# Kernel optimization log

Hardware: AMD Instinct MI355X
Metric: run time of the kernel (lower is better)

Reference implementation:

```python
import jax, jax.numpy as jnp
import numpy as np

B = 8          # batch of protein states
N = 20000      # num_nodes (atoms)
D = 640        # input_dim (latent per atom)
R = 2500       # number of residues (segments)
BINS = 10      # output_size_per_segment = (1, 10)
HID = 128      # decoder hidden dim
COND = 3       # conditioner_mode='X_ref' -> 3D reference coords
EPS = 1e-5     # BatchNorm1d eps


def _make_res_id():
    # ragged residue sizes cycling [6,8,10,8] -> exactly R residues, N atoms
    sizes = np.tile(np.array([6, 8, 10, 8], dtype=np.int64), R // 4)
    assert sizes.sum() == N
    return jnp.asarray(np.repeat(np.arange(R), sizes), dtype=jnp.int32)


def setup_inputs() -> dict:
    key = jax.random.key(0)
    ks = jax.random.split(key, 6)
    x = jax.random.normal(ks[0], (B * N, D), dtype=jnp.float32)
    conditioner = jax.random.normal(ks[1], (N, COND), dtype=jnp.float32)
    res_id = _make_res_id()  # [N] int32, sorted, atom -> residue
    W1 = jax.random.normal(ks[2], (BINS + COND, HID), dtype=jnp.float32) * 0.2
    b1 = jnp.zeros((HID,), jnp.float32)
    gamma = jnp.ones((HID,), jnp.float32)
    beta = jnp.zeros((HID,), jnp.float32)
    W2 = jax.random.normal(ks[3], (HID, 3), dtype=jnp.float32) * 0.1
    b2 = jnp.zeros((3,), jnp.float32)
    return {"x": x, "conditioner": conditioner, "res_id": res_id,
            "W1": W1, "b1": b1, "gamma": gamma, "beta": beta,
            "W2": W2, "b2": b2}


def reference(x, conditioner, res_id, W1, b1, gamma, beta, W2, b2):
    # x: [B*N, D] -> [B, N, D]
    x3 = x.reshape(B, N, D)

    # --- fused per-residue AdaptiveAvgPool2d((1,10)) ---
    # H-axis (atoms in residue) -> 1 : ragged segment mean via segment_sum
    counts = jax.ops.segment_sum(jnp.ones((N,), x.dtype), res_id,
                                 num_segments=R)                  # [R]
    seg_sum = jax.vmap(
        lambda xb: jax.ops.segment_sum(xb, res_id, num_segments=R)
    )(x3)                                                          # [B, R, D]
    seg_mean = seg_sum / counts[None, :, None]
    # W-axis: D -> 10 adaptive bins (exact since D % 10 == 0)
    pooled_latent = seg_mean.reshape(B, R, BINS, D // BINS).mean(-1)  # [B,R,10]

    # expand residue pooled vector back to its atoms, concat conditioner
    per_atom = pooled_latent[:, res_id, :]                        # [B, N, 10]
    cond = jnp.broadcast_to(conditioner[None], (B, N, COND))      # [B, N, 3]
    feat = jnp.concatenate([per_atom, cond], axis=-1).reshape(B * N, BINS + COND)

    # --- decoder MLP: Linear -> ReLU -> BatchNorm1d (train stats) -> Linear ---
    h = jax.nn.relu(feat @ W1 + b1)                               # [B*N, 128]
    mu = h.mean(axis=0)
    var = ((h - mu) ** 2).mean(axis=0)                            # biased, as torch BN
    hn = (h - mu) * jax.lax.rsqrt(var + EPS) * gamma + beta
    out = hn @ W2 + b2                                            # [B*N, 3]
    return out.reshape(B, N, 3)
```

## Files before the change

### kernel.cpp

```cpp
#include <hip/hip_runtime.h>

#define BB    8
#define NN    20000
#define DD    640
#define RR    2500
#define NBINS 10
#define HID   128
#define MTOT  (BB*NN)
#define SBLK  2048

__global__ void seg_bounds_kernel(const int* __restrict__ res_id,
                                  int* __restrict__ seg_start) {
    int r = blockIdx.x * blockDim.x + threadIdx.x;
    if (r > RR) return;
    if (r == RR) { seg_start[RR] = NN; return; }
    int lo = 0, hi = NN;
    while (lo < hi) {
        int mid = (lo + hi) >> 1;
        if (res_id[mid] < r) lo = mid + 1; else hi = mid;
    }
    seg_start[r] = lo;
}

__global__ __launch_bounds__(640) void pool_kernel(const float* __restrict__ x,
                                                   const int* __restrict__ seg_start,
                                                   float* __restrict__ pooled) {
    __shared__ float sbin[NBINS];
    int br = blockIdx.x;
    int b = br / RR;
    int r = br - b * RR;
    int t = threadIdx.x;
    if (t < NBINS) sbin[t] = 0.f;
    __syncthreads();

    int s0  = seg_start[r];
    int cnt = seg_start[r + 1] - s0;
    int nf4 = (cnt * DD) >> 2;
    const float4* xp = (const float4*)(x + (size_t)(b * NN + s0) * DD);

    float sum = 0.f;
    for (int idx = t; idx < nf4; idx += 640) {
        float4 v = xp[idx];
        sum += (v.x + v.y) + (v.z + v.w);
    }

    sum += __shfl_down(sum, 8, 16);
    sum += __shfl_down(sum, 4, 16);
    sum += __shfl_down(sum, 2, 16);
    sum += __shfl_down(sum, 1, 16);
    if ((t & 15) == 0) {
        int bin = ((t << 2) % DD) >> 6;
        atomicAdd(&sbin[bin], sum);
    }
    __syncthreads();
    if (t < NBINS) {
        float inv = cnt > 0 ? 1.f / (64.f * (float)cnt) : 0.f;
        pooled[(size_t)(b * RR + r) * NBINS + t] = sbin[t] * inv;
    }
}

__global__ __launch_bounds__(128) void stats_kernel(const float* __restrict__ pooled,
                                                    const float* __restrict__ cond,
                                                    const int* __restrict__ res_id,
                                                    const float* __restrict__ W1,
                                                    const float* __restrict__ b1,
                                                    float* __restrict__ partial) {
    int k = threadIdx.x;
    float w[13];
    #pragma unroll
    for (int j = 0; j < 13; j++) w[j] = W1[j * HID + k];
    float bk = b1[k];

    float s = 0.f, s2 = 0.f;
    for (int i = blockIdx.x; i < MTOT; i += SBLK) {
        int b = i / NN;
        int n = i - b * NN;
        int rid = res_id[n];
        const float* pr = pooled + (size_t)(b * RR + rid) * NBINS;
        const float* cr = cond + (size_t)n * 3;
        float h = bk;
        #pragma unroll
        for (int j = 0; j < NBINS; j++) h = fmaf(pr[j], w[j], h);
        h = fmaf(cr[0], w[10], h);
        h = fmaf(cr[1], w[11], h);
        h = fmaf(cr[2], w[12], h);
        h = fmaxf(h, 0.f);
        s += h;
        s2 = fmaf(h, h, s2);
    }
    partial[blockIdx.x * 256 + k]       = s;
    partial[blockIdx.x * 256 + 128 + k] = s2;
}

__global__ __launch_bounds__(1024) void finalize_kernel(const float* __restrict__ partial,
                                                        const float* __restrict__ gamma,
                                                        const float* __restrict__ beta,
                                                        const float* __restrict__ W2,
                                                        const float* __restrict__ b2,
                                                        float* __restrict__ W2eff,
                                                        float* __restrict__ b2eff) {
    int t = threadIdx.x;
    int slot = t & 255;
    int grp  = t >> 8;
    float acc = 0.f;
    for (int bi = grp; bi < SBLK; bi += 4) acc += partial[bi * 256 + slot];

    __shared__ float part4[4][256];
    __shared__ float contrib[HID * 3];
    part4[grp][slot] = acc;
    __syncthreads();

    if (t < HID) {
        float s  = part4[0][t] + part4[1][t] + part4[2][t] + part4[3][t];
        float s2 = part4[0][128 + t] + part4[1][128 + t] + part4[2][128 + t] + part4[3][128 + t];
        const float invM = 1.f / (float)MTOT;
        float mu  = s * invM;
        float var = fmaxf(s2 * invM - mu * mu, 0.f);
        float rs  = rsqrtf(var + 1e-5f);
        float sc  = gamma[t] * rs;
        float tk  = beta[t] - mu * sc;
        #pragma unroll
        for (int j = 0; j < 3; j++) {
            float wv = W2[t * 3 + j];
            W2eff[t * 3 + j]   = sc * wv;
            contrib[t * 3 + j] = tk * wv;
        }
    }
    __syncthreads();
    if (t < 3) {
        float a2 = b2[t];
        for (int kk = 0; kk < HID; kk++) a2 += contrib[kk * 3 + t];
        b2eff[t] = a2;
    }
}

__global__ __launch_bounds__(256) void out_kernel(const float* __restrict__ pooled,
                                                  const float* __restrict__ cond,
                                                  const int* __restrict__ res_id,
                                                  const float* __restrict__ W1,
                                                  const float* __restrict__ b1,
                                                  const float* __restrict__ W2eff,
                                                  const float* __restrict__ b2eff,
                                                  float* __restrict__ out) {
    int lane = threadIdx.x & 63;
    int wid  = (blockIdx.x * blockDim.x + threadIdx.x) >> 6;
    int nw   = (gridDim.x * blockDim.x) >> 6;
    int k1 = lane, k2 = lane + 64;

    float wa[13], wb[13];
    #pragma unroll
    for (int j = 0; j < 13; j++) {
        wa[j] = W1[j * HID + k1];
        wb[j] = W1[j * HID + k2];
    }
    float b1a = b1[k1], b1b = b1[k2];
    float wa0 = W2eff[k1 * 3 + 0], wa1 = W2eff[k1 * 3 + 1], wa2 = W2eff[k1 * 3 + 2];
    float wb0 = W2eff[k2 * 3 + 0], wb1 = W2eff[k2 * 3 + 1], wb2 = W2eff[k2 * 3 + 2];
    float e0 = b2eff[0], e1 = b2eff[1], e2 = b2eff[2];

    for (int i = wid; i < MTOT; i += nw) {
        int b = i / NN;
        int n = i - b * NN;
        int rid = res_id[n];
        const float* pr = pooled + (size_t)(b * RR + rid) * NBINS;
        const float* cr = cond + (size_t)n * 3;

        float h1 = b1a, h2 = b1b;
        #pragma unroll
        for (int j = 0; j < NBINS; j++) {
            h1 = fmaf(pr[j], wa[j], h1);
            h2 = fmaf(pr[j], wb[j], h2);
        }
        h1 = fmaf(cr[0], wa[10], h1); h1 = fmaf(cr[1], wa[11], h1); h1 = fmaf(cr[2], wa[12], h1);
        h2 = fmaf(cr[0], wb[10], h2); h2 = fmaf(cr[1], wb[11], h2); h2 = fmaf(cr[2], wb[12], h2);
        h1 = fmaxf(h1, 0.f);
        h2 = fmaxf(h2, 0.f);

        float p0 = h1 * wa0 + h2 * wb0;
        float p1 = h1 * wa1 + h2 * wb1;
        float p2 = h1 * wa2 + h2 * wb2;
        #pragma unroll
        for (int m = 1; m < 64; m <<= 1) {
            p0 += __shfl_xor(p0, m, 64);
            p1 += __shfl_xor(p1, m, 64);
            p2 += __shfl_xor(p2, m, 64);
        }
        if (lane == 0) {
            out[(size_t)i * 3 + 0] = p0 + e0;
            out[(size_t)i * 3 + 1] = p1 + e1;
            out[(size_t)i * 3 + 2] = p2 + e2;
        }
    }
}

extern "C" void kernel_launch(void* const* d_in, const int* in_sizes, int n_in,
                              void* d_out, int out_size, void* d_ws, size_t ws_size,
                              hipStream_t stream) {
    const float* x      = (const float*)d_in[0];
    const float* cond   = (const float*)d_in[1];
    const int*   res_id = (const int*)  d_in[2];
    const float* W1     = (const float*)d_in[3];
    const float* b1     = (const float*)d_in[4];
    const float* gamma  = (const float*)d_in[5];
    const float* beta   = (const float*)d_in[6];
    const float* W2     = (const float*)d_in[7];
    const float* b2     = (const float*)d_in[8];
    float* out = (float*)d_out;

    char* w = (char*)d_ws;
    int*   seg_start = (int*)  (w);
    float* pooled    = (float*)(w + 16384);
    float* partial   = (float*)(w + (1 << 20));
    float* W2eff     = (float*)(w + (3 << 20));
    float* b2eff     = (float*)(w + (3 << 20) + 4096);

    hipLaunchKernelGGL(seg_bounds_kernel, dim3(10), dim3(256), 0, stream,
                       res_id, seg_start);
    hipLaunchKernelGGL(pool_kernel, dim3(BB * RR), dim3(640), 0, stream,
                       x, seg_start, pooled);
    hipLaunchKernelGGL(stats_kernel, dim3(SBLK), dim3(128), 0, stream,
                       pooled, cond, res_id, W1, b1, partial);
    hipLaunchKernelGGL(finalize_kernel, dim3(1), dim3(1024), 0, stream,
                       partial, gamma, beta, W2, b2, W2eff, b2eff);
    hipLaunchKernelGGL(out_kernel, dim3(1024), dim3(256), 0, stream,
                       pooled, cond, res_id, W1, b1, W2eff, b2eff, out);
}
```

Baseline: 784.5 us.

## Map one row per thread in output MLP, fold segment bounds into pooling

The output kernel now assigns one atom row to each thread, with W1, W2eff and b1 staged in shared memory. Each thread recomputes the full 128-wide hidden layer itself, which removes the per-row 64-lane shuffle reductions and the 2/3-idle lane-0 stores. The separate segment-bounds kernel is removed; each pool block now binary-searches its own bounds, saving one launch at the cost of redundant searches. The stats grid also shrinks from 2048 to 1024 blocks, leaving fewer partials to reduce.

```diff
diff --git a/kernel.cpp b/kernel.cpp
--- a/kernel.cpp
+++ b/kernel.cpp
@@ -7,34 +7,32 @@
 #define NBINS 10
 #define HID   128
 #define MTOT  (BB*NN)
-#define SBLK  2048
-
-__global__ void seg_bounds_kernel(const int* __restrict__ res_id,
-                                  int* __restrict__ seg_start) {
-    int r = blockIdx.x * blockDim.x + threadIdx.x;
-    if (r > RR) return;
-    if (r == RR) { seg_start[RR] = NN; return; }
-    int lo = 0, hi = NN;
-    while (lo < hi) {
-        int mid = (lo + hi) >> 1;
-        if (res_id[mid] < r) lo = mid + 1; else hi = mid;
-    }
-    seg_start[r] = lo;
-}
+#define SBLK  1024
+#define OSTR  20
 
 __global__ __launch_bounds__(640) void pool_kernel(const float* __restrict__ x,
-                                                   const int* __restrict__ seg_start,
+                                                   const int* __restrict__ res_id,
                                                    float* __restrict__ pooled) {
     __shared__ float sbin[NBINS];
+    __shared__ int sbounds[2];
     int br = blockIdx.x;
     int b = br / RR;
     int r = br - b * RR;
     int t = threadIdx.x;
     if (t < NBINS) sbin[t] = 0.f;
-    __syncthreads();
-
-    int s0  = seg_start[r];
-    int cnt = seg_start[r + 1] - s0;
+    if (t < 2) {
+        int target = r + t;
+        int lo = 0, hi = NN;
+        while (lo < hi) {
+            int mid = (lo + hi) >> 1;
+            if (res_id[mid] < target) lo = mid + 1; else hi = mid;
+        }
+        sbounds[t] = lo;
+    }
+    __syncthreads();
+
+    int s0  = sbounds[0];
+    int cnt = sbounds[1] - s0;
     int nf4 = (cnt * DD) >> 2;
     const float4* xp = (const float4*)(x + (size_t)(b * NN + s0) * DD);
 
@@ -142,55 +140,47 @@
                                                   const float* __restrict__ W2eff,
                                                   const float* __restrict__ b2eff,
                                                   float* __restrict__ out) {
-    int lane = threadIdx.x & 63;
-    int wid  = (blockIdx.x * blockDim.x + threadIdx.x) >> 6;
-    int nw   = (gridDim.x * blockDim.x) >> 6;
-    int k1 = lane, k2 = lane + 64;
-
-    float wa[13], wb[13];
+    __shared__ float sw[HID * OSTR];
+    __shared__ float sb2[3];
+    int t = threadIdx.x;
+    for (int k = t; k < HID; k += 256) {
+        #pragma unroll
+        for (int j = 0; j < 13; j++) sw[k * OSTR + j] = W1[j * HID + k];
+        sw[k * OSTR + 13] = W2eff[k * 3 + 0];
+        sw[k * OSTR + 14] = W2eff[k * 3 + 1];
+        sw[k * OSTR + 15] = W2eff[k * 3 + 2];
+        sw[k * OSTR + 16] = b1[k];
+    }
+    if (t < 3) sb2[t] = b2eff[t];
+    __syncthreads();
+
+    int i = blockIdx.x * 256 + t;
+    int b = i / NN;
+    int n = i - b * NN;
+    int rid = res_id[n];
+    const float* pr = pooled + (size_t)(b * RR + rid) * NBINS;
+    const float* cr = cond + (size_t)n * 3;
+
+    float f[13];
     #pragma unroll
-    for (int j = 0; j < 13; j++) {
-        wa[j] = W1[j * HID + k1];
-        wb[j] = W1[j * HID + k2];
-    }
-    float b1a = b1[k1], b1b = b1[k2];
-    float wa0 = W2eff[k1 * 3 + 0], wa1 = W2eff[k1 * 3 + 1], wa2 = W2eff[k1 * 3 + 2];
-    float wb0 = W2eff[k2 * 3 + 0], wb1 = W2eff[k2 * 3 + 1], wb2 = W2eff[k2 * 3 + 2];
-    float e0 = b2eff[0], e1 = b2eff[1], e2 = b2eff[2];
-
-    for (int i = wid; i < MTOT; i += nw) {
-        int b = i / NN;
-        int n = i - b * NN;
-        int rid = res_id[n];
-        const float* pr = pooled + (size_t)(b * RR + rid) * NBINS;
-        const float* cr = cond + (size_t)n * 3;
-
-        float h1 = b1a, h2 = b1b;
-        #pragma unroll
-        for (int j = 0; j < NBINS; j++) {
-            h1 = fmaf(pr[j], wa[j], h1);
-            h2 = fmaf(pr[j], wb[j], h2);
-        }
-        h1 = fmaf(cr[0], wa[10], h1); h1 = fmaf(cr[1], wa[11], h1); h1 = fmaf(cr[2], wa[12], h1);
-        h2 = fmaf(cr[0], wb[10], h2); h2 = fmaf(cr[1], wb[11], h2); h2 = fmaf(cr[2], wb[12], h2);
-        h1 = fmaxf(h1, 0.f);
-        h2 = fmaxf(h2, 0.f);
-
-        float p0 = h1 * wa0 + h2 * wb0;
-        float p1 = h1 * wa1 + h2 * wb1;
-        float p2 = h1 * wa2 + h2 * wb2;
-        #pragma unroll
-        for (int m = 1; m < 64; m <<= 1) {
-            p0 += __shfl_xor(p0, m, 64);
-            p1 += __shfl_xor(p1, m, 64);
-            p2 += __shfl_xor(p2, m, 64);
-        }
-        if (lane == 0) {
-            out[(size_t)i * 3 + 0] = p0 + e0;
-            out[(size_t)i * 3 + 1] = p1 + e1;
-            out[(size_t)i * 3 + 2] = p2 + e2;
-        }
-    }
+    for (int j = 0; j < NBINS; j++) f[j] = pr[j];
+    f[10] = cr[0]; f[11] = cr[1]; f[12] = cr[2];
+
+    float o0 = sb2[0], o1 = sb2[1], o2 = sb2[2];
+    #pragma unroll 4
+    for (int k = 0; k < HID; k++) {
+        const float* wk = &sw[k * OSTR];
+        float h = wk[16];
+        #pragma unroll
+        for (int j = 0; j < 13; j++) h = fmaf(f[j], wk[j], h);
+        h = fmaxf(h, 0.f);
+        o0 = fmaf(h, wk[13], o0);
+        o1 = fmaf(h, wk[14], o1);
+        o2 = fmaf(h, wk[15], o2);
+    }
+    out[(size_t)i * 3 + 0] = o0;
+    out[(size_t)i * 3 + 1] = o1;
+    out[(size_t)i * 3 + 2] = o2;
 }
 
 extern "C" void kernel_launch(void* const* d_in, const int* in_sizes, int n_in,
@@ -208,20 +198,17 @@
     float* out = (float*)d_out;
 
     char* w = (char*)d_ws;
-    int*   seg_start = (int*)  (w);
     float* pooled    = (float*)(w + 16384);
     float* partial   = (float*)(w + (1 << 20));
     float* W2eff     = (float*)(w + (3 << 20));
     float* b2eff     = (float*)(w + (3 << 20) + 4096);
 
-    hipLaunchKernelGGL(seg_bounds_kernel, dim3(10), dim3(256), 0, stream,
-                       res_id, seg_start);
     hipLaunchKernelGGL(pool_kernel, dim3(BB * RR), dim3(640), 0, stream,
-                       x, seg_start, pooled);
+                       x, res_id, pooled);
     hipLaunchKernelGGL(stats_kernel, dim3(SBLK), dim3(128), 0, stream,
                        pooled, cond, res_id, W1, b1, partial);
     hipLaunchKernelGGL(finalize_kernel, dim3(1), dim3(1024), 0, stream,
                        partial, gamma, beta, W2, b2, W2eff, b2eff);
-    hipLaunchKernelGGL(out_kernel, dim3(1024), dim3(256), 0, stream,
+    hipLaunchKernelGGL(out_kernel, dim3(MTOT / 256), dim3(256), 0, stream,
                        pooled, cond, res_id, W1, b1, W2eff, b2eff, out);
 }
```

Result: slower. 805.7 us (+2.7%).
